# Optimization experiments

Measured on AMD Instinct MI355X. Metric: run time of the kernel, lower is better.

The kernel has to match this reference:

```python
import jax, jax.numpy as jnp
import numpy as np

N_NODES = 20000
LN_EPS = 1e-5


def setup_inputs() -> dict:
    key = jax.random.key(0)
    ks = jax.random.split(key, 8)
    N, E, D_IN, D_H = N_NODES, 320000, 128, 256
    x = jax.random.normal(ks[0], (N, D_IN), dtype=jnp.float32)
    edge_index = jax.random.randint(ks[1], (2, E), 0, N, dtype=jnp.int64)
    edge_weight = jax.random.uniform(ks[2], (E,), dtype=jnp.float32)
    # Glorot-ish scaled weights
    W1 = jax.random.normal(ks[3], (D_IN, D_H), dtype=jnp.float32) / np.sqrt(D_IN)
    W2 = jax.random.normal(ks[4], (D_H, D_H), dtype=jnp.float32) / np.sqrt(D_H)
    Wres = jax.random.normal(ks[5], (D_IN, D_H), dtype=jnp.float32) / np.sqrt(D_IN)
    return {
        "x": x, "edge_index": edge_index, "edge_weight": edge_weight,
        "W1": W1, "b1": jnp.zeros((D_H,), jnp.float32),
        "W2": W2, "b2": jnp.zeros((D_H,), jnp.float32),
        "Wres": Wres, "bres": jnp.zeros((D_H,), jnp.float32),
        "gamma1": jnp.ones((D_H,), jnp.float32), "beta1": jnp.zeros((D_H,), jnp.float32),
        "gamma2": jnp.ones((D_H,), jnp.float32), "beta2": jnp.zeros((D_H,), jnp.float32),
    }


def _gcn_conv(x, W, b, src, dst, w, n):
    # PyG GCNConv: linear transform, then sym-normalized scatter-add aggregation
    h = x @ W  # [N, D_H]
    deg = jax.ops.segment_sum(w, dst, num_segments=n)  # in-degree incl. self loops
    dinv = jnp.where(deg > 0, jax.lax.rsqrt(deg), 0.0)
    norm = dinv[src] * w * dinv[dst]  # [E+N]
    out = jax.ops.segment_sum(norm[:, None] * h[src], dst, num_segments=n)
    return out + b


def _layer_norm(x, gamma, beta):
    mu = jnp.mean(x, axis=-1, keepdims=True)
    var = jnp.mean(jnp.square(x - mu), axis=-1, keepdims=True)
    return (x - mu) * jax.lax.rsqrt(var + LN_EPS) * gamma + beta


def reference(x, edge_index, edge_weight, W1, b1, W2, b2, Wres, bres,
              gamma1, beta1, gamma2, beta2):
    n = x.shape[0]
    loop = jnp.arange(n, dtype=edge_index.dtype)
    # add self loops with weight 1 (add_self_loops=True)
    src = jnp.concatenate([edge_index[0], loop])
    dst = jnp.concatenate([edge_index[1], loop])
    w = jnp.concatenate([edge_weight, jnp.ones((n,), edge_weight.dtype)])

    # hop 0: conv -> relu (dropout p=0, eval) -> residual proj -> LayerNorm
    delta = jax.nn.relu(_gcn_conv(x, W1, b1, src, dst, w, n))
    h = _layer_norm(x @ Wres + bres + delta, gamma1, beta1)

    # hop 1 (last): conv -> residual -> LayerNorm (no relu)
    delta = _gcn_conv(h, W2, b2, src, dst, w, n)
    h = _layer_norm(h + delta, gamma2, beta2)
    return h
```

## Files before the change

kernel.cpp:

```cpp
#include <hip/hip_runtime.h>
#include <stdint.h>


constexpr int DIN = 128;
constexpr int DH  = 256;
#define LN_EPS 1e-5f

typedef __attribute__((ext_vector_type(8))) short bf16x8;
typedef __attribute__((ext_vector_type(4))) short bf16x4;
typedef __attribute__((ext_vector_type(4))) float f32x4;

__device__ __forceinline__ short f2bf(float f) {
  union { float f; unsigned u; } v; v.f = f;
  unsigned r = v.u + 0x7fffu + ((v.u >> 16) & 1u);
  return (short)(r >> 16);
}
__device__ __forceinline__ float bf2f(short b) {
  union { unsigned u; float f; } v; v.u = ((unsigned)(unsigned short)b) << 16;
  return v.f;
}

__device__ __forceinline__ int probe_m64(const unsigned* ei, int E) {
  int lane = threadIdx.x & 63;
  long long stride = (E >= 64) ? (E / 64) : 1;
  long long li = (long long)lane * stride;
  if (li >= E) li = 0;
  unsigned v = ei[2 * li + 1];
  return __ballot(v != 0u) == 0ull;
}

__device__ __forceinline__ int eidx(const void* ei, long long e, int m64) {
  return m64 ? (int)((const long long*)ei)[e] : ((const int*)ei)[e];
}


__global__ __launch_bounds__(256) void k_prep(const float* __restrict__ x,
                                              short* __restrict__ xb,
                                              const float* __restrict__ W1,
                                              const float* __restrict__ Wres,
                                              const float* __restrict__ W2,
                                              short* __restrict__ W1t,
                                              short* __restrict__ Wrt,
                                              short* __restrict__ W2t,
                                              const void* ei,
                                              const float* __restrict__ ew,
                                              float* deg, int* cnt,
                                              int N, int E) {
  const int NXV = N * DIN / 8;
  const int NW  = DIN * DH;
  const int NW2 = DH * DH;
  int idx = blockIdx.x * 256 + threadIdx.x;
  if (idx < NXV) {
    f32x4 a = ((const f32x4*)x)[idx * 2];
    f32x4 b = ((const f32x4*)x)[idx * 2 + 1];
    bf16x8 o;
    o[0] = f2bf(a[0]); o[1] = f2bf(a[1]); o[2] = f2bf(a[2]); o[3] = f2bf(a[3]);
    o[4] = f2bf(b[0]); o[5] = f2bf(b[1]); o[6] = f2bf(b[2]); o[7] = f2bf(b[3]);
    ((bf16x8*)xb)[idx] = o;
    return;
  }
  idx -= NXV;
  if (idx < NW) {
    int n = idx / DIN, k = idx % DIN;
    W1t[idx] = f2bf(W1[k * DH + n]);
    return;
  }
  idx -= NW;
  if (idx < NW) {
    int n = idx / DIN, k = idx % DIN;
    Wrt[idx] = f2bf(Wres[k * DH + n]);
    return;
  }
  idx -= NW;
  if (idx < NW2) {
    int n = idx / DH, k = idx % DH;
    W2t[idx] = f2bf(W2[k * DH + n]);
    return;
  }
  idx -= NW2;
  int m64 = probe_m64((const unsigned*)ei, E);
  if (idx < E) {
    int d = eidx(ei, (long long)E + idx, m64);
    atomicAdd(&deg[d], ew[idx]);
    atomicAdd(&cnt[d], 1);
  }
}


__global__ __launch_bounds__(1024) void k_scan(const int* __restrict__ cnt,
                                               float* deg, int* rowptr,
                                               int* cursor, int n) {
  for (int i = threadIdx.x; i < n; i += 1024) deg[i] = rsqrtf(1.0f + deg[i]);

  constexpr int MAXI = 32;
  int items = (n + 1023) / 1024;
  int tid = threadIdx.x, lane = tid & 63, wv = tid >> 6;
  int base = tid * items;
  int v[MAXI];
  int tot = 0;
#pragma unroll 4
  for (int j = 0; j < items; ++j) {
    int i = base + j;
    v[j] = (i < n) ? cnt[i] : 0;
    tot += v[j];
  }
  int sc = tot;
#pragma unroll
  for (int off = 1; off < 64; off <<= 1) {
    int t = __shfl_up(sc, off, 64);
    if (lane >= off) sc += t;
  }
  __shared__ int wsum[16];
  if (lane == 63) wsum[wv] = sc;
  __syncthreads();
  if (wv == 0 && lane < 16) {
    int s = wsum[lane];
#pragma unroll
    for (int off = 1; off < 16; off <<= 1) {
      int t = __shfl_up(s, off, 64);
      if (lane >= off) s += t;
    }
    wsum[lane] = s;
  }
  __syncthreads();
  int prefix = (sc - tot) + ((wv > 0) ? wsum[wv - 1] : 0);
  if (tid == 0) { rowptr[0] = 0; cursor[0] = 0; }
  int run = prefix;
#pragma unroll 4
  for (int j = 0; j < items; ++j) {
    int i = base + j;
    run += v[j];
    if (i < n) { rowptr[i + 1] = run; cursor[i + 1] = run; }
  }
}


__global__ __launch_bounds__(256) void k_fill(const void* ei,
                                              const float* __restrict__ w,
                                              const float* __restrict__ dinv,
                                              int* cursor, int* srcs,
                                              float* norms, int E) {
  int m64 = probe_m64((const unsigned*)ei, E);
  int e = blockIdx.x * 256 + threadIdx.x;
  if (e >= E) return;
  int s = eidx(ei, e, m64);
  int d = eidx(ei, (long long)E + e, m64);
  int p = atomicAdd(&cursor[d], 1);
  srcs[p] = s;
  norms[p] = dinv[s] * w[e] * dinv[d];
}


__global__ __launch_bounds__(256) void k_agg128(const short* __restrict__ T,
                                                const int* __restrict__ rowptr,
                                                const int* __restrict__ srcs,
                                                const float* __restrict__ norms,
                                                const float* __restrict__ dinv,
                                                short* __restrict__ out, int n) {
  int wv = threadIdx.x >> 6, lane = threadIdx.x & 63;
  int i = blockIdx.x * 4 + wv;
  if (i >= n) return;
  int h = lane >> 5;
  int c = (lane & 31) * 4;
  float a0 = 0.f, a1 = 0.f, a2 = 0.f, a3 = 0.f;
  int e = rowptr[i] + h, end = rowptr[i + 1];
  for (; e + 6 < end; e += 8) {
    int s0 = srcs[e], s1 = srcs[e + 2], s2 = srcs[e + 4], s3 = srcs[e + 6];
    float w0 = norms[e], w1 = norms[e + 2], w2 = norms[e + 4], w3 = norms[e + 6];
    bf16x4 v0 = *(const bf16x4*)(T + (long long)s0 * DIN + c);
    bf16x4 v1 = *(const bf16x4*)(T + (long long)s1 * DIN + c);
    bf16x4 v2 = *(const bf16x4*)(T + (long long)s2 * DIN + c);
    bf16x4 v3 = *(const bf16x4*)(T + (long long)s3 * DIN + c);
    a0 += w0 * bf2f(v0[0]) + w1 * bf2f(v1[0]) + w2 * bf2f(v2[0]) + w3 * bf2f(v3[0]);
    a1 += w0 * bf2f(v0[1]) + w1 * bf2f(v1[1]) + w2 * bf2f(v2[1]) + w3 * bf2f(v3[1]);
    a2 += w0 * bf2f(v0[2]) + w1 * bf2f(v1[2]) + w2 * bf2f(v2[2]) + w3 * bf2f(v3[2]);
    a3 += w0 * bf2f(v0[3]) + w1 * bf2f(v1[3]) + w2 * bf2f(v2[3]) + w3 * bf2f(v3[3]);
  }
  for (; e < end; e += 2) {
    int s = srcs[e];
    float w = norms[e];
    bf16x4 v = *(const bf16x4*)(T + (long long)s * DIN + c);
    a0 += w * bf2f(v[0]); a1 += w * bf2f(v[1]);
    a2 += w * bf2f(v[2]); a3 += w * bf2f(v[3]);
  }
  a0 += __shfl_xor(a0, 32, 64); a1 += __shfl_xor(a1, 32, 64);
  a2 += __shfl_xor(a2, 32, 64); a3 += __shfl_xor(a3, 32, 64);
  if (h == 0) {
    float sw = dinv[i] * dinv[i];
    bf16x4 sv = *(const bf16x4*)(T + (long long)i * DIN + c);
    bf16x4 o;
    o[0] = f2bf(a0 + sw * bf2f(sv[0]));
    o[1] = f2bf(a1 + sw * bf2f(sv[1]));
    o[2] = f2bf(a2 + sw * bf2f(sv[2]));
    o[3] = f2bf(a3 + sw * bf2f(sv[3]));
    *(bf16x4*)(out + (long long)i * DIN + c) = o;
  }
}

__global__ __launch_bounds__(256) void k_agg256(const short* __restrict__ T,
                                                const int* __restrict__ rowptr,
                                                const int* __restrict__ srcs,
                                                const float* __restrict__ norms,
                                                const float* __restrict__ dinv,
                                                short* __restrict__ out, int n) {
  int wv = threadIdx.x >> 6, lane = threadIdx.x & 63;
  int i = blockIdx.x * 4 + wv;
  if (i >= n) return;
  int h = lane >> 5;
  int c = (lane & 31) * 8;
  float acc[8];
#pragma unroll
  for (int k = 0; k < 8; ++k) acc[k] = 0.f;
  int e = rowptr[i] + h, end = rowptr[i + 1];
  for (; e + 6 < end; e += 8) {
    int s0 = srcs[e], s1 = srcs[e + 2], s2 = srcs[e + 4], s3 = srcs[e + 6];
    float w0 = norms[e], w1 = norms[e + 2], w2 = norms[e + 4], w3 = norms[e + 6];
    bf16x8 v0 = *(const bf16x8*)(T + (long long)s0 * DH + c);
    bf16x8 v1 = *(const bf16x8*)(T + (long long)s1 * DH + c);
    bf16x8 v2 = *(const bf16x8*)(T + (long long)s2 * DH + c);
    bf16x8 v3 = *(const bf16x8*)(T + (long long)s3 * DH + c);
#pragma unroll
    for (int k = 0; k < 8; ++k)
      acc[k] += w0 * bf2f(v0[k]) + w1 * bf2f(v1[k]) +
                w2 * bf2f(v2[k]) + w3 * bf2f(v3[k]);
  }
  for (; e < end; e += 2) {
    int s = srcs[e];
    float w = norms[e];
    bf16x8 v = *(const bf16x8*)(T + (long long)s * DH + c);
#pragma unroll
    for (int k = 0; k < 8; ++k) acc[k] += w * bf2f(v[k]);
  }
#pragma unroll
  for (int k = 0; k < 8; ++k) acc[k] += __shfl_xor(acc[k], 32, 64);
  if (h == 0) {
    float sw = dinv[i] * dinv[i];
    bf16x8 sv = *(const bf16x8*)(T + (long long)i * DH + c);
    bf16x8 o;
#pragma unroll
    for (int k = 0; k < 8; ++k) o[k] = f2bf(acc[k] + sw * bf2f(sv[k]));
    *(bf16x8*)(out + (long long)i * DH + c) = o;
  }
}


__global__ __launch_bounds__(256) void k_gemm_ln1(
    const short* __restrict__ Sx, const short* __restrict__ xb,
    const short* __restrict__ W1t, const short* __restrict__ Wrt,
    const float* __restrict__ b1, const float* __restrict__ bres,
    const float* __restrict__ g1, const float* __restrict__ be1,
    short* __restrict__ h1b, int M) {
  __shared__ short As[16][DIN + 8];
  __shared__ short Xs[16][DIN + 8];
  __shared__ float red1[4][16], red2[4][16];
  int tid = threadIdx.x;
  int wv = tid >> 6, lane = tid & 63;
  int lr = lane & 15, lg = lane >> 4;
  int bm = blockIdx.x * 16;

  {
    int row = tid >> 4, ch = tid & 15;
    int gr = min(bm + row, M - 1);
    *(bf16x8*)(&As[row][ch * 8]) = *(const bf16x8*)(Sx + (long long)gr * DIN + ch * 8);
    *(bf16x8*)(&Xs[row][ch * 8]) = *(const bf16x8*)(xb + (long long)gr * DIN + ch * 8);
  }
  __syncthreads();

  f32x4 acc[4] = {};
#pragma unroll
  for (int ks = 0; ks < 4; ++ks) {
    bf16x8 a = *(const bf16x8*)(&As[lr][ks * 32 + lg * 8]);
#pragma unroll
    for (int ni = 0; ni < 4; ++ni) {
      int col = (wv * 4 + ni) * 16 + lr;
      bf16x8 b = *(const bf16x8*)(W1t + col * DIN + ks * 32 + lg * 8);
      acc[ni] = __builtin_amdgcn_mfma_f32_16x16x32_bf16(a, b, acc[ni], 0, 0, 0);
    }
  }
#pragma unroll
  for (int ni = 0; ni < 4; ++ni) {
    int col = (wv * 4 + ni) * 16 + lr;
    float bb = b1[col], br = bres[col];
#pragma unroll
    for (int j = 0; j < 4; ++j)
      acc[ni][j] = fmaxf(acc[ni][j] + bb, 0.f) + br;
  }
#pragma unroll
  for (int ks = 0; ks < 4; ++ks) {
    bf16x8 a = *(const bf16x8*)(&Xs[lr][ks * 32 + lg * 8]);
#pragma unroll
    for (int ni = 0; ni < 4; ++ni) {
      int col = (wv * 4 + ni) * 16 + lr;
      bf16x8 b = *(const bf16x8*)(Wrt + col * DIN + ks * 32 + lg * 8);
      acc[ni] = __builtin_amdgcn_mfma_f32_16x16x32_bf16(a, b, acc[ni], 0, 0, 0);
    }
  }
#pragma unroll
  for (int j = 0; j < 4; ++j) {
    float s1 = acc[0][j] + acc[1][j] + acc[2][j] + acc[3][j];
    float s2 = acc[0][j] * acc[0][j] + acc[1][j] * acc[1][j] +
               acc[2][j] * acc[2][j] + acc[3][j] * acc[3][j];
#pragma unroll
    for (int m = 1; m < 16; m <<= 1) {
      s1 += __shfl_xor(s1, m, 64);
      s2 += __shfl_xor(s2, m, 64);
    }
    if (lr == 0) { red1[wv][lg * 4 + j] = s1; red2[wv][lg * 4 + j] = s2; }
  }
  __syncthreads();
#pragma unroll
  for (int j = 0; j < 4; ++j) {
    int row = lg * 4 + j;
    float s1 = red1[0][row] + red1[1][row] + red1[2][row] + red1[3][row];
    float s2 = red2[0][row] + red2[1][row] + red2[2][row] + red2[3][row];
    float mu = s1 * (1.f / 256.f);
    float rs = rsqrtf(s2 * (1.f / 256.f) - mu * mu + LN_EPS);
    int r = bm + row;
    if (r < M) {
#pragma unroll
      for (int ni = 0; ni < 4; ++ni) {
        int col = (wv * 4 + ni) * 16 + lr;
        float y = (acc[ni][j] - mu) * rs * g1[col] + be1[col];
        h1b[(long long)r * DH + col] = f2bf(y);
      }
    }
  }
}


__global__ __launch_bounds__(256) void k_gemm_ln2(
    const short* __restrict__ Sh1, const short* __restrict__ h1b,
    const short* __restrict__ W2t, const float* __restrict__ b2,
    const float* __restrict__ g2, const float* __restrict__ be2,
    float* __restrict__ out, int M) {
  __shared__ short As[16][DH + 8];
  __shared__ short Hs[16][DH + 8];
  __shared__ float red1[4][16], red2[4][16];
  int tid = threadIdx.x;
  int wv = tid >> 6, lane = tid & 63;
  int lr = lane & 15, lg = lane >> 4;
  int bm = blockIdx.x * 16;

  {
#pragma unroll
    for (int q = 0; q < 2; ++q) {
      int cidx = q * 256 + tid;
      int row = cidx >> 5, ch = cidx & 31;
      int gr = min(bm + row, M - 1);
      *(bf16x8*)(&As[row][ch * 8]) = *(const bf16x8*)(Sh1 + (long long)gr * DH + ch * 8);
      *(bf16x8*)(&Hs[row][ch * 8]) = *(const bf16x8*)(h1b + (long long)gr * DH + ch * 8);
    }
  }
  __syncthreads();

  f32x4 acc[4] = {};
#pragma unroll
  for (int ks = 0; ks < 8; ++ks) {
    bf16x8 a = *(const bf16x8*)(&As[lr][ks * 32 + lg * 8]);
#pragma unroll
    for (int ni = 0; ni < 4; ++ni) {
      int col = (wv * 4 + ni) * 16 + lr;
      bf16x8 b = *(const bf16x8*)(W2t + col * DH + ks * 32 + lg * 8);
      acc[ni] = __builtin_amdgcn_mfma_f32_16x16x32_bf16(a, b, acc[ni], 0, 0, 0);
    }
  }
#pragma unroll
  for (int j = 0; j < 4; ++j) {
    int row = lg * 4 + j;
#pragma unroll
    for (int ni = 0; ni < 4; ++ni) {
      int col = (wv * 4 + ni) * 16 + lr;
      acc[ni][j] += b2[col] + bf2f(Hs[row][col]);
    }
  }
#pragma unroll
  for (int j = 0; j < 4; ++j) {
    float s1 = acc[0][j] + acc[1][j] + acc[2][j] + acc[3][j];
    float s2 = acc[0][j] * acc[0][j] + acc[1][j] * acc[1][j] +
               acc[2][j] * acc[2][j] + acc[3][j] * acc[3][j];
#pragma unroll
    for (int m = 1; m < 16; m <<= 1) {
      s1 += __shfl_xor(s1, m, 64);
      s2 += __shfl_xor(s2, m, 64);
    }
    if (lr == 0) { red1[wv][lg * 4 + j] = s1; red2[wv][lg * 4 + j] = s2; }
  }
  __syncthreads();
#pragma unroll
  for (int j = 0; j < 4; ++j) {
    int row = lg * 4 + j;
    float s1 = red1[0][row] + red1[1][row] + red1[2][row] + red1[3][row];
    float s2 = red2[0][row] + red2[1][row] + red2[2][row] + red2[3][row];
    float mu = s1 * (1.f / 256.f);
    float rs = rsqrtf(s2 * (1.f / 256.f) - mu * mu + LN_EPS);
    int r = bm + row;
    if (r < M) {
#pragma unroll
      for (int ni = 0; ni < 4; ++ni) {
        int col = (wv * 4 + ni) * 16 + lr;
        out[(long long)r * DH + col] = (acc[ni][j] - mu) * rs * g2[col] + be2[col];
      }
    }
  }
}


extern "C" void kernel_launch(void* const* d_in, const int* in_sizes, int n_in,
                              void* d_out, int out_size, void* d_ws,
                              size_t ws_size, hipStream_t stream) {
  const float* x    = (const float*)d_in[0];
  const void*  ei   = d_in[1];
  const float* ew   = (const float*)d_in[2];
  const float* W1   = (const float*)d_in[3];
  const float* b1   = (const float*)d_in[4];
  const float* W2   = (const float*)d_in[5];
  const float* b2   = (const float*)d_in[6];
  const float* Wres = (const float*)d_in[7];
  const float* bres = (const float*)d_in[8];
  const float* g1   = (const float*)d_in[9];
  const float* be1  = (const float*)d_in[10];
  const float* g2   = (const float*)d_in[11];
  const float* be2  = (const float*)d_in[12];

  const int N = in_sizes[0] / DIN;
  const int E = in_sizes[2];

  char* ws = (char*)d_ws;
  auto alloc = [&](size_t bytes) -> char* {
    char* p = ws;
    ws += (bytes + 255) & ~(size_t)255;
    return p;
  };
  short* xb     = (short*)alloc((size_t)N * DIN * 2);
  short* W1t    = (short*)alloc((size_t)DIN * DH * 2);
  short* Wrt    = (short*)alloc((size_t)DIN * DH * 2);
  short* W2t    = (short*)alloc((size_t)DH * DH * 2);
  short* Sx     = (short*)alloc((size_t)N * DIN * 2);
  short* h1b    = (short*)alloc((size_t)N * DH * 2);
  short* Sh1    = (short*)alloc((size_t)N * DH * 2);
  int*   cnt    = (int*)alloc((size_t)N * 8);
  float* deg    = (float*)(cnt + N);
  int*   rowptr = (int*)alloc((size_t)(N + 1) * 4);
  int*   cursor = (int*)alloc((size_t)(N + 1) * 4);
  int*   srcs   = (int*)alloc((size_t)E * 4);
  float* norms  = (float*)alloc((size_t)E * 4);

  hipMemsetAsync(cnt, 0, (size_t)N * 8, stream);

  int prep_items = N * DIN / 8 + 2 * DIN * DH + DH * DH + E;
  k_prep<<<(prep_items + 255) / 256, 256, 0, stream>>>(
      x, xb, W1, Wres, W2, W1t, Wrt, W2t, ei, ew, deg, cnt, N, E);
  k_scan<<<1, 1024, 0, stream>>>(cnt, deg, rowptr, cursor, N);
  k_fill<<<(E + 255) / 256, 256, 0, stream>>>(ei, ew, deg, cursor, srcs, norms, E);

  k_agg128<<<(N + 3) / 4, 256, 0, stream>>>(xb, rowptr, srcs, norms, deg, Sx, N);
  const int NB = (N + 15) / 16;
  k_gemm_ln1<<<NB, 256, 0, stream>>>(Sx, xb, W1t, Wrt, b1, bres, g1, be1,
                                     h1b, N);
  k_agg256<<<(N + 3) / 4, 256, 0, stream>>>(h1b, rowptr, srcs, norms, deg, Sh1, N);
  k_gemm_ln2<<<NB, 256, 0, stream>>>(Sh1, h1b, W2t, b2, g2, be2,
                                     (float*)d_out, N);
}
```

Measured before the change: 261.7 us.

## Fuse neighbor aggregation into GEMM+LayerNorm kernels via shared memory

```diff
diff --git a/kernel.cpp b/kernel.cpp
--- a/kernel.cpp
+++ b/kernel.cpp
@@ -151,105 +151,13 @@
 }
 
 
-__global__ __launch_bounds__(256) void k_agg128(const short* __restrict__ T,
-                                                const int* __restrict__ rowptr,
-                                                const int* __restrict__ srcs,
-                                                const float* __restrict__ norms,
-                                                const float* __restrict__ dinv,
-                                                short* __restrict__ out, int n) {
-  int wv = threadIdx.x >> 6, lane = threadIdx.x & 63;
-  int i = blockIdx.x * 4 + wv;
-  if (i >= n) return;
-  int h = lane >> 5;
-  int c = (lane & 31) * 4;
-  float a0 = 0.f, a1 = 0.f, a2 = 0.f, a3 = 0.f;
-  int e = rowptr[i] + h, end = rowptr[i + 1];
-  for (; e + 6 < end; e += 8) {
-    int s0 = srcs[e], s1 = srcs[e + 2], s2 = srcs[e + 4], s3 = srcs[e + 6];
-    float w0 = norms[e], w1 = norms[e + 2], w2 = norms[e + 4], w3 = norms[e + 6];
-    bf16x4 v0 = *(const bf16x4*)(T + (long long)s0 * DIN + c);
-    bf16x4 v1 = *(const bf16x4*)(T + (long long)s1 * DIN + c);
-    bf16x4 v2 = *(const bf16x4*)(T + (long long)s2 * DIN + c);
-    bf16x4 v3 = *(const bf16x4*)(T + (long long)s3 * DIN + c);
-    a0 += w0 * bf2f(v0[0]) + w1 * bf2f(v1[0]) + w2 * bf2f(v2[0]) + w3 * bf2f(v3[0]);
-    a1 += w0 * bf2f(v0[1]) + w1 * bf2f(v1[1]) + w2 * bf2f(v2[1]) + w3 * bf2f(v3[1]);
-    a2 += w0 * bf2f(v0[2]) + w1 * bf2f(v1[2]) + w2 * bf2f(v2[2]) + w3 * bf2f(v3[2]);
-    a3 += w0 * bf2f(v0[3]) + w1 * bf2f(v1[3]) + w2 * bf2f(v2[3]) + w3 * bf2f(v3[3]);
-  }
-  for (; e < end; e += 2) {
-    int s = srcs[e];
-    float w = norms[e];
-    bf16x4 v = *(const bf16x4*)(T + (long long)s * DIN + c);
-    a0 += w * bf2f(v[0]); a1 += w * bf2f(v[1]);
-    a2 += w * bf2f(v[2]); a3 += w * bf2f(v[3]);
-  }
-  a0 += __shfl_xor(a0, 32, 64); a1 += __shfl_xor(a1, 32, 64);
-  a2 += __shfl_xor(a2, 32, 64); a3 += __shfl_xor(a3, 32, 64);
-  if (h == 0) {
-    float sw = dinv[i] * dinv[i];
-    bf16x4 sv = *(const bf16x4*)(T + (long long)i * DIN + c);
-    bf16x4 o;
-    o[0] = f2bf(a0 + sw * bf2f(sv[0]));
-    o[1] = f2bf(a1 + sw * bf2f(sv[1]));
-    o[2] = f2bf(a2 + sw * bf2f(sv[2]));
-    o[3] = f2bf(a3 + sw * bf2f(sv[3]));
-    *(bf16x4*)(out + (long long)i * DIN + c) = o;
-  }
-}
-
-__global__ __launch_bounds__(256) void k_agg256(const short* __restrict__ T,
-                                                const int* __restrict__ rowptr,
-                                                const int* __restrict__ srcs,
-                                                const float* __restrict__ norms,
-                                                const float* __restrict__ dinv,
-                                                short* __restrict__ out, int n) {
-  int wv = threadIdx.x >> 6, lane = threadIdx.x & 63;
-  int i = blockIdx.x * 4 + wv;
-  if (i >= n) return;
-  int h = lane >> 5;
-  int c = (lane & 31) * 8;
-  float acc[8];
-#pragma unroll
-  for (int k = 0; k < 8; ++k) acc[k] = 0.f;
-  int e = rowptr[i] + h, end = rowptr[i + 1];
-  for (; e + 6 < end; e += 8) {
-    int s0 = srcs[e], s1 = srcs[e + 2], s2 = srcs[e + 4], s3 = srcs[e + 6];
-    float w0 = norms[e], w1 = norms[e + 2], w2 = norms[e + 4], w3 = norms[e + 6];
-    bf16x8 v0 = *(const bf16x8*)(T + (long long)s0 * DH + c);
-    bf16x8 v1 = *(const bf16x8*)(T + (long long)s1 * DH + c);
-    bf16x8 v2 = *(const bf16x8*)(T + (long long)s2 * DH + c);
-    bf16x8 v3 = *(const bf16x8*)(T + (long long)s3 * DH + c);
-#pragma unroll
-    for (int k = 0; k < 8; ++k)
-      acc[k] += w0 * bf2f(v0[k]) + w1 * bf2f(v1[k]) +
-                w2 * bf2f(v2[k]) + w3 * bf2f(v3[k]);
-  }
-  for (; e < end; e += 2) {
-    int s = srcs[e];
-    float w = norms[e];
-    bf16x8 v = *(const bf16x8*)(T + (long long)s * DH + c);
-#pragma unroll
-    for (int k = 0; k < 8; ++k) acc[k] += w * bf2f(v[k]);
-  }
-#pragma unroll
-  for (int k = 0; k < 8; ++k) acc[k] += __shfl_xor(acc[k], 32, 64);
-  if (h == 0) {
-    float sw = dinv[i] * dinv[i];
-    bf16x8 sv = *(const bf16x8*)(T + (long long)i * DH + c);
-    bf16x8 o;
-#pragma unroll
-    for (int k = 0; k < 8; ++k) o[k] = f2bf(acc[k] + sw * bf2f(sv[k]));
-    *(bf16x8*)(out + (long long)i * DH + c) = o;
-  }
-}
-
-
-__global__ __launch_bounds__(256) void k_gemm_ln1(
-    const short* __restrict__ Sx, const short* __restrict__ xb,
-    const short* __restrict__ W1t, const short* __restrict__ Wrt,
-    const float* __restrict__ b1, const float* __restrict__ bres,
-    const float* __restrict__ g1, const float* __restrict__ be1,
-    short* __restrict__ h1b, int M) {
+__global__ __launch_bounds__(256) void k_layer1(
+    const short* __restrict__ xb, const short* __restrict__ W1t,
+    const short* __restrict__ Wrt, const float* __restrict__ b1,
+    const float* __restrict__ bres, const float* __restrict__ g1,
+    const float* __restrict__ be1, const int* __restrict__ rowptr,
+    const int* __restrict__ srcs, const float* __restrict__ norms,
+    const float* __restrict__ dinv, short* __restrict__ h1b, int M) {
   __shared__ short As[16][DIN + 8];
   __shared__ short Xs[16][DIN + 8];
   __shared__ float red1[4][16], red2[4][16];
@@ -261,8 +169,50 @@
   {
     int row = tid >> 4, ch = tid & 15;
     int gr = min(bm + row, M - 1);
-    *(bf16x8*)(&As[row][ch * 8]) = *(const bf16x8*)(Sx + (long long)gr * DIN + ch * 8);
     *(bf16x8*)(&Xs[row][ch * 8]) = *(const bf16x8*)(xb + (long long)gr * DIN + ch * 8);
+  }
+
+  {
+    int h = lane >> 5;
+    int c = (lane & 31) * 4;
+#pragma unroll
+    for (int rr = 0; rr < 4; ++rr) {
+      int r = wv * 4 + rr;
+      int i = min(bm + r, M - 1);
+      float a0 = 0.f, a1 = 0.f, a2 = 0.f, a3 = 0.f;
+      int e = rowptr[i] + h, end = rowptr[i + 1];
+      for (; e + 6 < end; e += 8) {
+        int s0 = srcs[e], s1 = srcs[e + 2], s2 = srcs[e + 4], s3 = srcs[e + 6];
+        float w0 = norms[e], w1 = norms[e + 2], w2 = norms[e + 4], w3 = norms[e + 6];
+        bf16x4 v0 = *(const bf16x4*)(xb + (long long)s0 * DIN + c);
+        bf16x4 v1 = *(const bf16x4*)(xb + (long long)s1 * DIN + c);
+        bf16x4 v2 = *(const bf16x4*)(xb + (long long)s2 * DIN + c);
+        bf16x4 v3 = *(const bf16x4*)(xb + (long long)s3 * DIN + c);
+        a0 += w0 * bf2f(v0[0]) + w1 * bf2f(v1[0]) + w2 * bf2f(v2[0]) + w3 * bf2f(v3[0]);
+        a1 += w0 * bf2f(v0[1]) + w1 * bf2f(v1[1]) + w2 * bf2f(v2[1]) + w3 * bf2f(v3[1]);
+        a2 += w0 * bf2f(v0[2]) + w1 * bf2f(v1[2]) + w2 * bf2f(v2[2]) + w3 * bf2f(v3[2]);
+        a3 += w0 * bf2f(v0[3]) + w1 * bf2f(v1[3]) + w2 * bf2f(v2[3]) + w3 * bf2f(v3[3]);
+      }
+      for (; e < end; e += 2) {
+        int s = srcs[e];
+        float w = norms[e];
+        bf16x4 v = *(const bf16x4*)(xb + (long long)s * DIN + c);
+        a0 += w * bf2f(v[0]); a1 += w * bf2f(v[1]);
+        a2 += w * bf2f(v[2]); a3 += w * bf2f(v[3]);
+      }
+      a0 += __shfl_xor(a0, 32, 64); a1 += __shfl_xor(a1, 32, 64);
+      a2 += __shfl_xor(a2, 32, 64); a3 += __shfl_xor(a3, 32, 64);
+      if (h == 0) {
+        float sw = dinv[i] * dinv[i];
+        bf16x4 sv = *(const bf16x4*)(xb + (long long)i * DIN + c);
+        bf16x4 o;
+        o[0] = f2bf(a0 + sw * bf2f(sv[0]));
+        o[1] = f2bf(a1 + sw * bf2f(sv[1]));
+        o[2] = f2bf(a2 + sw * bf2f(sv[2]));
+        o[3] = f2bf(a3 + sw * bf2f(sv[3]));
+        *(bf16x4*)(&As[r][c]) = o;
+      }
+    }
   }
   __syncthreads();
 
@@ -328,11 +278,12 @@
 }
 
 
-__global__ __launch_bounds__(256) void k_gemm_ln2(
-    const short* __restrict__ Sh1, const short* __restrict__ h1b,
-    const short* __restrict__ W2t, const float* __restrict__ b2,
-    const float* __restrict__ g2, const float* __restrict__ be2,
-    float* __restrict__ out, int M) {
+__global__ __launch_bounds__(256) void k_layer2(
+    const short* __restrict__ h1b, const short* __restrict__ W2t,
+    const float* __restrict__ b2, const float* __restrict__ g2,
+    const float* __restrict__ be2, const int* __restrict__ rowptr,
+    const int* __restrict__ srcs, const float* __restrict__ norms,
+    const float* __restrict__ dinv, float* __restrict__ out, int M) {
   __shared__ short As[16][DH + 8];
   __shared__ short Hs[16][DH + 8];
   __shared__ float red1[4][16], red2[4][16];
@@ -347,8 +298,50 @@
       int cidx = q * 256 + tid;
       int row = cidx >> 5, ch = cidx & 31;
       int gr = min(bm + row, M - 1);
-      *(bf16x8*)(&As[row][ch * 8]) = *(const bf16x8*)(Sh1 + (long long)gr * DH + ch * 8);
       *(bf16x8*)(&Hs[row][ch * 8]) = *(const bf16x8*)(h1b + (long long)gr * DH + ch * 8);
+    }
+  }
+
+  {
+    int h = lane >> 5;
+    int c = (lane & 31) * 8;
+#pragma unroll
+    for (int rr = 0; rr < 4; ++rr) {
+      int r = wv * 4 + rr;
+      int i = min(bm + r, M - 1);
+      float acc[8];
+#pragma unroll
+      for (int k = 0; k < 8; ++k) acc[k] = 0.f;
+      int e = rowptr[i] + h, end = rowptr[i + 1];
+      for (; e + 6 < end; e += 8) {
+        int s0 = srcs[e], s1 = srcs[e + 2], s2 = srcs[e + 4], s3 = srcs[e + 6];
+        float w0 = norms[e], w1 = norms[e + 2], w2 = norms[e + 4], w3 = norms[e + 6];
+        bf16x8 v0 = *(const bf16x8*)(h1b + (long long)s0 * DH + c);
+        bf16x8 v1 = *(const bf16x8*)(h1b + (long long)s1 * DH + c);
+        bf16x8 v2 = *(const bf16x8*)(h1b + (long long)s2 * DH + c);
+        bf16x8 v3 = *(const bf16x8*)(h1b + (long long)s3 * DH + c);
+#pragma unroll
+        for (int k = 0; k < 8; ++k)
+          acc[k] += w0 * bf2f(v0[k]) + w1 * bf2f(v1[k]) +
+                    w2 * bf2f(v2[k]) + w3 * bf2f(v3[k]);
+      }
+      for (; e < end; e += 2) {
+        int s = srcs[e];
+        float w = norms[e];
+        bf16x8 v = *(const bf16x8*)(h1b + (long long)s * DH + c);
+#pragma unroll
+        for (int k = 0; k < 8; ++k) acc[k] += w * bf2f(v[k]);
+      }
+#pragma unroll
+      for (int k = 0; k < 8; ++k) acc[k] += __shfl_xor(acc[k], 32, 64);
+      if (h == 0) {
+        float sw = dinv[i] * dinv[i];
+        bf16x8 sv = *(const bf16x8*)(h1b + (long long)i * DH + c);
+        bf16x8 o;
+#pragma unroll
+        for (int k = 0; k < 8; ++k) o[k] = f2bf(acc[k] + sw * bf2f(sv[k]));
+        *(bf16x8*)(&As[r][c]) = o;
+      }
     }
   }
   __syncthreads();
@@ -435,9 +428,7 @@
   short* W1t    = (short*)alloc((size_t)DIN * DH * 2);
   short* Wrt    = (short*)alloc((size_t)DIN * DH * 2);
   short* W2t    = (short*)alloc((size_t)DH * DH * 2);
-  short* Sx     = (short*)alloc((size_t)N * DIN * 2);
   short* h1b    = (short*)alloc((size_t)N * DH * 2);
-  short* Sh1    = (short*)alloc((size_t)N * DH * 2);
   int*   cnt    = (int*)alloc((size_t)N * 8);
   float* deg    = (float*)(cnt + N);
   int*   rowptr = (int*)alloc((size_t)(N + 1) * 4);
@@ -453,11 +444,9 @@
   k_scan<<<1, 1024, 0, stream>>>(cnt, deg, rowptr, cursor, N);
   k_fill<<<(E + 255) / 256, 256, 0, stream>>>(ei, ew, deg, cursor, srcs, norms, E);
 
-  k_agg128<<<(N + 3) / 4, 256, 0, stream>>>(xb, rowptr, srcs, norms, deg, Sx, N);
   const int NB = (N + 15) / 16;
-  k_gemm_ln1<<<NB, 256, 0, stream>>>(Sx, xb, W1t, Wrt, b1, bres, g1, be1,
-                                     h1b, N);
-  k_agg256<<<(N + 3) / 4, 256, 0, stream>>>(h1b, rowptr, srcs, norms, deg, Sh1, N);
-  k_gemm_ln2<<<NB, 256, 0, stream>>>(Sh1, h1b, W2t, b2, g2, be2,
-                                     (float*)d_out, N);
-}
+  k_layer1<<<NB, 256, 0, stream>>>(xb, W1t, Wrt, b1, bres, g1, be1, rowptr,
+                                   srcs, norms, deg, h1b, N);
+  k_layer2<<<NB, 256, 0, stream>>>(h1b, W2t, b2, g2, be2, rowptr, srcs, norms,
+                                   deg, (float*)d_out, N);
+}
```

New measurement: 273.8 us. 1.05x slower.
